# Kernel optimization log

Hardware: AMD Instinct MI355X
Metric: run time of the kernel (lower is better)

The kernel has to match this reference:

```python
import jax, jax.numpy as jnp
import numpy as np

N, IN_DIM, OUT_DIM, H = 8192, 512, 512, 1
BN_EPS = 1e-5


def _lin(key, fan_in, fan_out):
    k1, k2 = jax.random.split(key)
    b = 1.0 / np.sqrt(fan_in)
    W = jax.random.uniform(k1, (fan_in, fan_out), jnp.float32, -b, b)
    bias = jax.random.uniform(k2, (fan_out,), jnp.float32, -b, b)
    return W, bias


def setup_inputs() -> dict:
    key = jax.random.key(0)
    ks = jax.random.split(key, 12)
    h = jax.random.normal(ks[0], (N, IN_DIM), jnp.float32)
    A = (jax.random.uniform(ks[1], (N, N)) < 0.01).astype(jnp.float32)
    qw, qb = _lin(ks[2], IN_DIM, OUT_DIM * H)
    kw, kb = _lin(ks[3], IN_DIM, OUT_DIM * H)
    vw, vb = _lin(ks[4], IN_DIM, OUT_DIM * H)
    ow, ob = _lin(ks[5], OUT_DIM, OUT_DIM)
    f1w, f1b = _lin(ks[6], OUT_DIM, OUT_DIM * 2)
    f2w, f2b = _lin(ks[7], OUT_DIM * 2, OUT_DIM)
    bn1_g = jax.random.normal(ks[8], (OUT_DIM,)) * 0.1 + 1.0
    bn1_b = jax.random.normal(ks[9], (OUT_DIM,)) * 0.1
    bn1_m = jax.random.normal(ks[10], (OUT_DIM,)) * 0.1
    bn1_v = jax.random.uniform(ks[11], (OUT_DIM,), jnp.float32, 0.5, 1.5)
    ks2 = jax.random.split(jax.random.fold_in(key, 7), 4)
    bn2_g = jax.random.normal(ks2[0], (OUT_DIM,)) * 0.1 + 1.0
    bn2_b = jax.random.normal(ks2[1], (OUT_DIM,)) * 0.1
    bn2_m = jax.random.normal(ks2[2], (OUT_DIM,)) * 0.1
    bn2_v = jax.random.uniform(ks2[3], (OUT_DIM,), jnp.float32, 0.5, 1.5)
    return dict(A=A, h=h, qw=qw, qb=qb, kw=kw, kb=kb, vw=vw, vb=vb,
                ow=ow, ob=ob, f1w=f1w, f1b=f1b, f2w=f2w, f2b=f2b,
                bn1_g=bn1_g, bn1_b=bn1_b, bn1_m=bn1_m, bn1_v=bn1_v,
                bn2_g=bn2_g, bn2_b=bn2_b, bn2_m=bn2_m, bn2_v=bn2_v)


def _bn_eval(x, g, b, m, v):
    return (x - m) * jax.lax.rsqrt(v + BN_EPS) * g + b


def reference(A, h, qw, qb, kw, kb, vw, vb, ow, ob, f1w, f1b, f2w, f2b,
              bn1_g, bn1_b, bn1_m, bn1_v, bn2_g, bn2_b, bn2_m, bn2_v):
    n = h.shape[0]
    scaling = OUT_DIM ** (-0.5)
    # q/k/v: [N, D, H] as in torch reshape of [N, D*H]
    q = (h @ qw + qb).reshape(n, OUT_DIM, H) * scaling
    k = (h @ kw + kb).reshape(n, OUT_DIM, H)
    v = (h @ vw + vb).reshape(n, OUT_DIM, H)
    qh = jnp.transpose(q, (2, 0, 1))          # (H, N, D)
    kh = jnp.transpose(k, (2, 1, 0))          # (H, D, N)
    vh = jnp.transpose(v, (2, 0, 1))          # (H, N, D)
    attn = jnp.einsum('hnd,hdm->hnm', qh, kh) * A[None]   # (H, N, N)
    attn = jax.nn.softmax(attn, axis=0)        # NOTE: softmax over HEAD axis, as in source
    out = jnp.einsum('hnm,hmd->hnd', attn, vh).reshape(n, H * OUT_DIM)
    # GTLayer (eval mode: dropout = identity, BN uses running stats)
    x = out @ ow + ob
    x = x + h                                  # residual
    x = _bn_eval(x, bn1_g, bn1_b, bn1_m, bn1_v)
    h2 = x
    f = jax.nn.relu(x @ f1w + f1b) @ f2w + f2b
    x = h2 + f
    x = _bn_eval(x, bn2_g, bn2_b, bn2_m, bn2_v)
    return x
```

## Files before the change

kernel.cpp:

```cpp
#include <hip/hip_runtime.h>

#define NROWS 8192
#define DIM 512
#define HID 1024
#define BN_EPS 1e-5f

typedef unsigned short ushort_t;
typedef __attribute__((ext_vector_type(8))) __bf16 bf16x8;
typedef __attribute__((ext_vector_type(4))) float f32x4;

union U4 {
    uint4 u;
    bf16x8 b;
    ushort_t s[8];
};

static __device__ __forceinline__ float b2f(ushort_t u) {
    union { float f; unsigned int i; } c;
    c.i = ((unsigned int)u) << 16;
    return c.f;
}

static __device__ __forceinline__ ushort_t f2b(float f) {
    union { float f; unsigned int i; } c;
    c.f = f;
    unsigned int i = c.i;
    unsigned int r = (i + 0x7FFFu + ((i >> 16) & 1u)) >> 16;
    return (ushort_t)r;
}

static __device__ __forceinline__ void gload_lds16(const ushort_t* g, ushort_t* l) {
    __builtin_amdgcn_global_load_lds((const __attribute__((address_space(1))) void*)g,
                                     (__attribute__((address_space(3))) void*)l, 16, 0, 0);
}

__global__ void colsum_kernel(const float* __restrict__ h, float* __restrict__ hs) {
    __shared__ float red[512];
    int t = threadIdx.x;
    int col0 = (t & 127) * 4;
    int rsub = t >> 7;
    int row0 = blockIdx.x * 32;
    float acc[4] = {0.f, 0.f, 0.f, 0.f};
#pragma unroll
    for (int r = 0; r < 16; ++r) {
        int row = row0 + r * 2 + rsub;
        float4 v = *(const float4*)(h + (size_t)row * DIM + col0);
        acc[0] += v.x; acc[1] += v.y; acc[2] += v.z; acc[3] += v.w;
    }
    if (rsub) {
#pragma unroll
        for (int j = 0; j < 4; ++j) red[col0 + j] = acc[j];
    }
    __syncthreads();
    if (!rsub) {
#pragma unroll
        for (int j = 0; j < 4; ++j) atomicAdd(&hs[col0 + j], acc[j] + red[col0 + j]);
    }
}

__global__ void matvec_kernel(const float* __restrict__ xin, const float* __restrict__ W,
                              const float* __restrict__ bvec, float scaleB,
                              float* __restrict__ outv) {
    __shared__ float red[8][32];
    int t = threadIdx.x;
    int col = blockIdx.x * 32 + (t & 31);
    int ks = t >> 5;
    float s = 0.f;
    for (int ki = 0; ki < 64; ++ki) {
        int k = ks * 64 + ki;
        s += xin[k] * W[k * 512 + col];
    }
    red[ks][t & 31] = s;
    __syncthreads();
    if (ks == 0) {
        float tot = scaleB * bvec[col];
#pragma unroll
        for (int r = 0; r < 8; ++r) tot += red[r][t & 31];
        outv[col] = tot;
    }
}

__global__ void matvec_prep_kernel(const float* __restrict__ xin, const float* __restrict__ W,
                                   const float* __restrict__ bvec,
                                   const float* g1, const float* b1,
                                   const float* m1, const float* v1,
                                   const float* g2, const float* b2,
                                   const float* m2, const float* v2,
                                   float* __restrict__ p, float* __restrict__ q0,
                                   float* __restrict__ a2v, float* __restrict__ c2v) {
    __shared__ float red[8][32];
    int t = threadIdx.x;
    int col = blockIdx.x * 32 + (t & 31);
    int ks = t >> 5;
    float s = 0.f;
    for (int ki = 0; ki < 64; ++ki) {
        int k = ks * 64 + ki;
        s += xin[k] * W[k * 512 + col];
    }
    red[ks][t & 31] = s;
    __syncthreads();
    if (ks == 0) {
        float tot = bvec[col];
#pragma unroll
        for (int r = 0; r < 8; ++r) tot += red[r][t & 31];
        float a1 = g1[col] * rsqrtf(v1[col] + BN_EPS);
        float c1 = b1[col] - m1[col] * a1;
        p[col] = a1;
        q0[col] = tot * a1 + c1;
        float a2 = g2[col] * rsqrtf(v2[col] + BN_EPS);
        a2v[col] = a2;
        c2v[col] = b2[col] - m2[col] * a2;
    }
}

__global__ void x1_kernel(const float* __restrict__ h, const float* __restrict__ p,
                          const float* __restrict__ q0, ushort_t* __restrict__ x1) {
    int idx = (blockIdx.x * blockDim.x + threadIdx.x) * 8;
    int d0 = idx & (DIM - 1);
    float4 h0 = *(const float4*)(h + idx);
    float4 h1 = *(const float4*)(h + idx + 4);
    U4 o;
    o.s[0] = f2b(h0.x * p[d0 + 0] + q0[d0 + 0]);
    o.s[1] = f2b(h0.y * p[d0 + 1] + q0[d0 + 1]);
    o.s[2] = f2b(h0.z * p[d0 + 2] + q0[d0 + 2]);
    o.s[3] = f2b(h0.w * p[d0 + 3] + q0[d0 + 3]);
    o.s[4] = f2b(h1.x * p[d0 + 4] + q0[d0 + 4]);
    o.s[5] = f2b(h1.y * p[d0 + 5] + q0[d0 + 5]);
    o.s[6] = f2b(h1.z * p[d0 + 6] + q0[d0 + 6]);
    o.s[7] = f2b(h1.w * p[d0 + 7] + q0[d0 + 7]);
    *(uint4*)(x1 + idx) = o.u;
}

__global__ void transpose_kernel(const float* __restrict__ in, ushort_t* __restrict__ out,
                                 int R, int C) {
    __shared__ float tile[32][33];
    int tx = threadIdx.x & 31, ty = threadIdx.x >> 5;
    int bx = blockIdx.x * 32, by = blockIdx.y * 32;
#pragma unroll
    for (int i = 0; i < 32; i += 8)
        tile[ty + i][tx] = in[(by + ty + i) * C + bx + tx];
    __syncthreads();
#pragma unroll
    for (int i = 0; i < 32; i += 8)
        out[(bx + ty + i) * R + by + tx] = f2b(tile[tx][ty + i]);
}

template <int ROWS>
static __device__ __forceinline__ void stage_tile(const ushort_t* __restrict__ g, int ldg,
                                                  ushort_t* lds, int tid) {
#pragma unroll
    for (int it = 0; it < (ROWS * 8) / 256; ++it) {
        int c = it * 256 + tid;
        int row = c >> 3;
        int kc = (c & 7) << 3;
        const ushort_t* gp = g + (size_t)row * ldg + kc;
        ushort_t* lp = lds + ((it * 256 + (tid & 192)) << 3);
        gload_lds16(gp, lp);
    }
}

template <int NJ, bool RELU, bool FUSE>
__global__ __launch_bounds__(256) void gemm_kernel(
    const ushort_t* __restrict__ A, const ushort_t* __restrict__ BT,
    const float* __restrict__ bias, ushort_t* __restrict__ Cb,
    float* __restrict__ Cf, int M, int Nn, int K,
    const float* __restrict__ h, const float* __restrict__ p,
    const float* __restrict__ q0, const float* __restrict__ a2,
    const float* __restrict__ c2) {
    constexpr int BN = NJ * 32;
    constexpr int BK = 64;
    __shared__ ushort_t As[128 * BK];
    __shared__ ushort_t Bs[BN * BK];
    int tid = threadIdx.x;
    int lane = tid & 63, w = tid >> 6;
    int wm = (w & 1) * 64, wn = (w >> 1) * (NJ * 16);
    int bm = blockIdx.y * 128, bn = blockIdx.x * BN;

    f32x4 acc[4][NJ] = {};

    const ushort_t* Ag = A + (size_t)bm * K;
    const ushort_t* Bg = BT + (size_t)bn * K;

    for (int k0 = 0; k0 < K; k0 += BK) {
        __syncthreads();
        stage_tile<128>(Ag + k0, K, As, tid);
        stage_tile<BN>(Bg + k0, K, Bs, tid);
        __syncthreads();
#pragma unroll
        for (int ks = 0; ks < 2; ++ks) {
            int koff = ks * 32 + (lane >> 4) * 8;
            bf16x8 af[4], bfr[NJ];
#pragma unroll
            for (int i = 0; i < 4; ++i) {
                U4 t;
                t.u = *(const uint4*)(As + (wm + i * 16 + (lane & 15)) * BK + koff);
                af[i] = t.b;
            }
#pragma unroll
            for (int j = 0; j < NJ; ++j) {
                U4 t;
                t.u = *(const uint4*)(Bs + (wn + j * 16 + (lane & 15)) * BK + koff);
                bfr[j] = t.b;
            }
#pragma unroll
            for (int i = 0; i < 4; ++i)
#pragma unroll
                for (int j = 0; j < NJ; ++j)
                    acc[i][j] = __builtin_amdgcn_mfma_f32_16x16x32_bf16(af[i], bfr[j], acc[i][j], 0, 0, 0);
        }
    }

#pragma unroll
    for (int i = 0; i < 4; ++i) {
        int row0 = bm + wm + i * 16 + (lane >> 4) * 4;
#pragma unroll
        for (int j = 0; j < NJ; ++j) {
            int col = bn + wn + j * 16 + (lane & 15);
            float bv = bias[col];
            if constexpr (FUSE) {
                float pv = p[col], qv = q0[col], av = a2[col], cv = c2[col];
#pragma unroll
                for (int r = 0; r < 4; ++r) {
                    int row = row0 + r;
                    float hv = h[(size_t)row * DIM + col];
                    float x1v = hv * pv + qv;
                    Cf[(size_t)row * Nn + col] = (x1v + acc[i][j][r] + bv) * av + cv;
                }
            } else {
#pragma unroll
                for (int r = 0; r < 4; ++r) {
                    float v = acc[i][j][r] + bv;
                    if (RELU) v = fmaxf(v, 0.f);
                    Cb[(size_t)(row0 + r) * Nn + col] = f2b(v);
                }
            }
        }
    }
}

extern "C" void kernel_launch(void* const* d_in, const int* in_sizes, int n_in,
                              void* d_out, int out_size, void* d_ws, size_t ws_size,
                              hipStream_t stream) {
    const float* h = (const float*)d_in[1];
    const float* vw = (const float*)d_in[6];
    const float* vb = (const float*)d_in[7];
    const float* ow = (const float*)d_in[8];
    const float* ob = (const float*)d_in[9];
    const float* f1w = (const float*)d_in[10];
    const float* f1b = (const float*)d_in[11];
    const float* f2w = (const float*)d_in[12];
    const float* f2b = (const float*)d_in[13];
    const float* g1 = (const float*)d_in[14];
    const float* b1 = (const float*)d_in[15];
    const float* m1 = (const float*)d_in[16];
    const float* v1 = (const float*)d_in[17];
    const float* g2 = (const float*)d_in[18];
    const float* b2 = (const float*)d_in[19];
    const float* m2 = (const float*)d_in[20];
    const float* v2 = (const float*)d_in[21];
    float* out = (float*)d_out;

    char* ws = (char*)d_ws;
    float* hs = (float*)(ws + 0);
    float* pC = (float*)(ws + 2048);
    float* q0C = (float*)(ws + 4096);
    float* a2C = (float*)(ws + 6144);
    float* c2C = (float*)(ws + 8192);
    float* sBuf = (float*)(ws + 10240);
    ushort_t* X1 = (ushort_t*)(ws + 16384);
    ushort_t* Z = X1 + (size_t)NROWS * DIM;
    ushort_t* W1T = Z + (size_t)NROWS * HID;
    ushort_t* W2T = W1T + (size_t)HID * DIM;

    hipMemsetAsync(hs, 0, 512 * sizeof(float), stream);
    colsum_kernel<<<256, 256, 0, stream>>>(h, hs);
    matvec_kernel<<<16, 256, 0, stream>>>(hs, vw, vb, 8192.0f, sBuf);
    matvec_prep_kernel<<<16, 256, 0, stream>>>(sBuf, ow, ob, g1, b1, m1, v1,
                                               g2, b2, m2, v2, pC, q0C, a2C, c2C);
    x1_kernel<<<2048, 256, 0, stream>>>(h, pC, q0C, X1);
    transpose_kernel<<<dim3(32, 16), 256, 0, stream>>>(f1w, W1T, 512, 1024);
    transpose_kernel<<<dim3(16, 32), 256, 0, stream>>>(f2w, W2T, 1024, 512);
    gemm_kernel<4, true, false><<<dim3(8, 64), 256, 0, stream>>>(
        X1, W1T, f1b, Z, nullptr, NROWS, HID, DIM,
        nullptr, nullptr, nullptr, nullptr, nullptr);
    gemm_kernel<2, false, true><<<dim3(8, 64), 256, 0, stream>>>(
        Z, W2T, f2b, nullptr, out, NROWS, DIM, HID,
        h, pC, q0C, a2C, c2C);
}
```

Before: 434.3 us.

## Fuse x1 normalization into GEMM A-staging and merge prep and transpose launches

Removes the x1 kernel by having the first GEMM read fp32 h directly, apply the BN1 affine and convert to bf16 while staging the A tile into shared memory. The two matvec kernels become one, with each block redundantly computing the full first matvec. The two weight transposes become a single launch. This cuts launches and the X1 round trip through memory, but the A-tile load is now a synchronous register path instead of an async global-to-LDS copy, and the fp32 reads double A bytes per tile.

```diff
diff --git a/kernel.cpp b/kernel.cpp
--- a/kernel.cpp
+++ b/kernel.cpp
@@ -58,49 +58,38 @@
     }
 }
 
-__global__ void matvec_kernel(const float* __restrict__ xin, const float* __restrict__ W,
-                              const float* __restrict__ bvec, float scaleB,
-                              float* __restrict__ outv) {
+__global__ void chainprep_kernel(const float* __restrict__ hs,
+                                 const float* __restrict__ vw, const float* __restrict__ vb,
+                                 const float* __restrict__ ow, const float* __restrict__ ob,
+                                 const float* g1, const float* b1,
+                                 const float* m1, const float* v1,
+                                 const float* g2, const float* b2,
+                                 const float* m2, const float* v2,
+                                 float* __restrict__ p, float* __restrict__ q0,
+                                 float* __restrict__ a2v, float* __restrict__ c2v) {
+    __shared__ float sS[512];
     __shared__ float red[8][32];
     int t = threadIdx.x;
+    float acc0 = 0.f, acc1 = 0.f;
+    for (int k = 0; k < 512; ++k) {
+        float hv = hs[k];
+        acc0 += hv * vw[k * 512 + t];
+        acc1 += hv * vw[k * 512 + t + 256];
+    }
+    sS[t] = acc0 + 8192.0f * vb[t];
+    sS[t + 256] = acc1 + 8192.0f * vb[t + 256];
+    __syncthreads();
     int col = blockIdx.x * 32 + (t & 31);
     int ks = t >> 5;
-    float s = 0.f;
+    float s2 = 0.f;
     for (int ki = 0; ki < 64; ++ki) {
         int k = ks * 64 + ki;
-        s += xin[k] * W[k * 512 + col];
-    }
-    red[ks][t & 31] = s;
+        s2 += sS[k] * ow[k * 512 + col];
+    }
+    red[ks][t & 31] = s2;
     __syncthreads();
     if (ks == 0) {
-        float tot = scaleB * bvec[col];
-#pragma unroll
-        for (int r = 0; r < 8; ++r) tot += red[r][t & 31];
-        outv[col] = tot;
-    }
-}
-
-__global__ void matvec_prep_kernel(const float* __restrict__ xin, const float* __restrict__ W,
-                                   const float* __restrict__ bvec,
-                                   const float* g1, const float* b1,
-                                   const float* m1, const float* v1,
-                                   const float* g2, const float* b2,
-                                   const float* m2, const float* v2,
-                                   float* __restrict__ p, float* __restrict__ q0,
-                                   float* __restrict__ a2v, float* __restrict__ c2v) {
-    __shared__ float red[8][32];
-    int t = threadIdx.x;
-    int col = blockIdx.x * 32 + (t & 31);
-    int ks = t >> 5;
-    float s = 0.f;
-    for (int ki = 0; ki < 64; ++ki) {
-        int k = ks * 64 + ki;
-        s += xin[k] * W[k * 512 + col];
-    }
-    red[ks][t & 31] = s;
-    __syncthreads();
-    if (ks == 0) {
-        float tot = bvec[col];
+        float tot = ob[col];
 #pragma unroll
         for (int r = 0; r < 8; ++r) tot += red[r][t & 31];
         float a1 = g1[col] * rsqrtf(v1[col] + BN_EPS);
@@ -113,29 +102,22 @@
     }
 }
 
-__global__ void x1_kernel(const float* __restrict__ h, const float* __restrict__ p,
-                          const float* __restrict__ q0, ushort_t* __restrict__ x1) {
-    int idx = (blockIdx.x * blockDim.x + threadIdx.x) * 8;
-    int d0 = idx & (DIM - 1);
-    float4 h0 = *(const float4*)(h + idx);
-    float4 h1 = *(const float4*)(h + idx + 4);
-    U4 o;
-    o.s[0] = f2b(h0.x * p[d0 + 0] + q0[d0 + 0]);
-    o.s[1] = f2b(h0.y * p[d0 + 1] + q0[d0 + 1]);
-    o.s[2] = f2b(h0.z * p[d0 + 2] + q0[d0 + 2]);
-    o.s[3] = f2b(h0.w * p[d0 + 3] + q0[d0 + 3]);
-    o.s[4] = f2b(h1.x * p[d0 + 4] + q0[d0 + 4]);
-    o.s[5] = f2b(h1.y * p[d0 + 5] + q0[d0 + 5]);
-    o.s[6] = f2b(h1.z * p[d0 + 6] + q0[d0 + 6]);
-    o.s[7] = f2b(h1.w * p[d0 + 7] + q0[d0 + 7]);
-    *(uint4*)(x1 + idx) = o.u;
-}
-
-__global__ void transpose_kernel(const float* __restrict__ in, ushort_t* __restrict__ out,
-                                 int R, int C) {
+__global__ void transpose_both_kernel(const float* __restrict__ f1w, ushort_t* __restrict__ W1T,
+                                      const float* __restrict__ f2w, ushort_t* __restrict__ W2T) {
     __shared__ float tile[32][33];
+    int bid = blockIdx.x;
+    const float* in;
+    ushort_t* out;
+    int R, C, bx, by;
+    if (bid < 512) {
+        in = f1w; out = W1T; R = 512; C = 1024;
+        bx = (bid & 31) * 32; by = (bid >> 5) * 32;
+    } else {
+        int b = bid - 512;
+        in = f2w; out = W2T; R = 1024; C = 512;
+        bx = (b & 15) * 32; by = (b >> 4) * 32;
+    }
     int tx = threadIdx.x & 31, ty = threadIdx.x >> 5;
-    int bx = blockIdx.x * 32, by = blockIdx.y * 32;
 #pragma unroll
     for (int i = 0; i < 32; i += 8)
         tile[ty + i][tx] = in[(by + ty + i) * C + bx + tx];
@@ -159,9 +141,10 @@
     }
 }
 
-template <int NJ, bool RELU, bool FUSE>
+template <int NJ, bool RELU, bool FUSE, bool AH>
 __global__ __launch_bounds__(256) void gemm_kernel(
-    const ushort_t* __restrict__ A, const ushort_t* __restrict__ BT,
+    const ushort_t* __restrict__ A, const float* __restrict__ Ah,
+    const ushort_t* __restrict__ BT,
     const float* __restrict__ bias, ushort_t* __restrict__ Cb,
     float* __restrict__ Cf, int M, int Nn, int K,
     const float* __restrict__ h, const float* __restrict__ p,
@@ -183,7 +166,24 @@
 
     for (int k0 = 0; k0 < K; k0 += BK) {
         __syncthreads();
-        stage_tile<128>(Ag + k0, K, As, tid);
+        if constexpr (AH) {
+#pragma unroll
+            for (int it = 0; it < 8; ++it) {
+                int c = it * 256 + tid;
+                int row = c >> 4, q = (c & 15) * 4;
+                float4 hv = *(const float4*)(Ah + (size_t)(bm + row) * K + k0 + q);
+                float4 pv = *(const float4*)(p + k0 + q);
+                float4 qv = *(const float4*)(q0 + k0 + q);
+                ushort_t o[4];
+                o[0] = f2b(hv.x * pv.x + qv.x);
+                o[1] = f2b(hv.y * pv.y + qv.y);
+                o[2] = f2b(hv.z * pv.z + qv.z);
+                o[3] = f2b(hv.w * pv.w + qv.w);
+                *(uint2*)(As + row * BK + q) = *(uint2*)o;
+            }
+        } else {
+            stage_tile<128>(Ag + k0, K, As, tid);
+        }
         stage_tile<BN>(Bg + k0, K, Bs, tid);
         __syncthreads();
 #pragma unroll
@@ -266,24 +266,20 @@
     float* q0C = (float*)(ws + 4096);
     float* a2C = (float*)(ws + 6144);
     float* c2C = (float*)(ws + 8192);
-    float* sBuf = (float*)(ws + 10240);
-    ushort_t* X1 = (ushort_t*)(ws + 16384);
-    ushort_t* Z = X1 + (size_t)NROWS * DIM;
+    ushort_t* Z = (ushort_t*)(ws + 16384);
     ushort_t* W1T = Z + (size_t)NROWS * HID;
     ushort_t* W2T = W1T + (size_t)HID * DIM;
 
     hipMemsetAsync(hs, 0, 512 * sizeof(float), stream);
     colsum_kernel<<<256, 256, 0, stream>>>(h, hs);
-    matvec_kernel<<<16, 256, 0, stream>>>(hs, vw, vb, 8192.0f, sBuf);
-    matvec_prep_kernel<<<16, 256, 0, stream>>>(sBuf, ow, ob, g1, b1, m1, v1,
-                                               g2, b2, m2, v2, pC, q0C, a2C, c2C);
-    x1_kernel<<<2048, 256, 0, stream>>>(h, pC, q0C, X1);
-    transpose_kernel<<<dim3(32, 16), 256, 0, stream>>>(f1w, W1T, 512, 1024);
-    transpose_kernel<<<dim3(16, 32), 256, 0, stream>>>(f2w, W2T, 1024, 512);
-    gemm_kernel<4, true, false><<<dim3(8, 64), 256, 0, stream>>>(
-        X1, W1T, f1b, Z, nullptr, NROWS, HID, DIM,
-        nullptr, nullptr, nullptr, nullptr, nullptr);
-    gemm_kernel<2, false, true><<<dim3(8, 64), 256, 0, stream>>>(
-        Z, W2T, f2b, nullptr, out, NROWS, DIM, HID,
+    chainprep_kernel<<<16, 256, 0, stream>>>(hs, vw, vb, ow, ob,
+                                             g1, b1, m1, v1, g2, b2, m2, v2,
+                                             pC, q0C, a2C, c2C);
+    transpose_both_kernel<<<1024, 256, 0, stream>>>(f1w, W1T, f2w, W2T);
+    gemm_kernel<4, true, false, true><<<dim3(8, 64), 256, 0, stream>>>(
+        nullptr, h, W1T, f1b, Z, nullptr, NROWS, HID, DIM,
+        nullptr, pC, q0C, nullptr, nullptr);
+    gemm_kernel<2, false, true, false><<<dim3(8, 64), 256, 0, stream>>>(
+        Z, nullptr, W2T, f2b, nullptr, out, NROWS, DIM, HID,
         h, pC, q0C, a2C, c2C);
 }
```

Result: slower. 460.3 us (+6.0%).
